# Performance work log

Measured on AMD Instinct MI355X. Metric: run time of the kernel, lower is better.

Reference implementation:

```python
import jax, jax.numpy as jnp
import numpy as np

B, T, N, K = 8, 1024, 64, 8


def _normalize_logprob(logmat, axis):
    # temperature = 1 in forward_backward
    norm = jax.scipy.special.logsumexp(logmat, axis=axis, keepdims=True)
    return logmat - norm, norm


def setup_inputs() -> dict:
    key = jax.random.key(0)
    k1, k2, k3 = jax.random.split(key, 3)
    log_a = jax.random.normal(k1, (B, T, N, K, K), dtype=jnp.float32)
    log_b = jax.random.normal(k2, (B, T, N, K), dtype=jnp.float32)
    logprob_z1 = jax.random.normal(k3, (N, K), dtype=jnp.float32)
    return {"log_a": log_a, "log_b": log_b, "logprob_z1": logprob_z1}


def reference(log_a, log_b, logprob_z1):
    # log_a: (B,T,N,K,K)  transition log-probs a[t][i,j] = p(z_t=i | z_{t-1}=j)
    # log_b: (B,T,N,K)    emission log-likelihoods
    # logprob_z1: (N,K)   initial state log-prob (Z_init parameter)
    b_tm = jnp.moveaxis(log_b, 1, 0)  # (T,B,N,K) time-major for scan
    a_tm = jnp.moveaxis(log_a, 1, 0)  # (T,B,N,K,K)

    # ---- forward recursion ----
    alpha0, norm0 = _normalize_logprob(logprob_z1[None] + log_b[:, 0], -1)  # (B,N,K),(B,N,1)

    def fstep(prev, xs):
        b_t, a_t = xs  # (B,N,K), (B,N,K,K)
        # alpha_t[i] = logsumexp_j( b_t[i] + a_t[i,j] + prev[j] )
        u = jax.scipy.special.logsumexp(
            b_t[..., :, None] + a_t + prev[..., None, :], axis=-1)
        alpha, nrm = _normalize_logprob(u, -1)
        return alpha, (alpha, nrm)

    _, (alphas, fnorms) = jax.lax.scan(fstep, alpha0, (b_tm[1:], a_tm[1:]))
    forward_probs = jnp.moveaxis(
        jnp.concatenate([alpha0[None], alphas], axis=0), 0, 1)  # (B,T,N,K)

    # ---- backward recursion ----
    betaT = jnp.zeros_like(alpha0)  # (B,N,K)

    def bstep(nxt, xs):
        b_tp1, a_tp1 = xs  # (B,N,K), (B,N,K,K)
        # beta_t[j] = logsumexp_i( nxt[i] + a_tp1[i,j] + b_tp1[i] )
        u = jax.scipy.special.logsumexp(
            nxt[..., :, None] + a_tp1 + b_tp1[..., :, None], axis=-2)
        beta, nrm = _normalize_logprob(u, -1)
        return beta, (beta, nrm)

    _, (betas, bnorms) = jax.lax.scan(
        bstep, betaT, (b_tm[1:], a_tm[1:]), reverse=True)
    backward_probs = jnp.moveaxis(
        jnp.concatenate([betas, betaT[None]], axis=0), 0, 1)  # (B,T,N,K)

    # ---- posteriors ----
    gamma1, _ = _normalize_logprob(forward_probs + backward_probs, -1)  # (B,T,N,K)

    # gamma2[t][i,j] ~ beta_t[i] + a_t[i,j] + b_t[i] + alpha_{t-1}[j], t >= 1
    g2u = (forward_probs[:, :-1, :, None, :]      # (B,T-1,N,1,K)
           + backward_probs[:, 1:, :, :, None]    # (B,T-1,N,K,1)
           + log_a[:, 1:]                         # (B,T-1,N,K,K)
           + log_b[:, 1:][..., None])             # (B,T-1,N,K,1)
    g2_norm = jax.scipy.special.logsumexp(g2u, axis=(-2, -1), keepdims=True)
    gamma2_unpad = g2u - g2_norm
    gamma2 = jnp.concatenate(
        [jnp.zeros_like(gamma2_unpad[:, :1]), gamma2_unpad], axis=1)  # (B,T,N,K,K)

    return forward_probs, backward_probs, gamma1, gamma2
```

## Files before the change

### kernel.cpp

```cpp
#include <hip/hip_runtime.h>

#define Tdim 1024
#define Ndim 64
#define FSZ (8 * 1024 * 64 * 8)

typedef unsigned uint2v __attribute__((ext_vector_type(2)));

#define DPPADD(v, ctrl) ((v) + __int_as_float(__builtin_amdgcn_update_dpp( \
    0, __float_as_int(v), ctrl, 0xF, 0xF, false)))

__device__ __forceinline__ float swap_add16(float v) {
  unsigned u = __float_as_uint(v);
  uint2v r = __builtin_amdgcn_permlane16_swap(u, u, false, false);
  return __uint_as_float(r[0]) + __uint_as_float(r[1]);
}
__device__ __forceinline__ float swap_add32(float v) {
  unsigned u = __float_as_uint(v);
  uint2v r = __builtin_amdgcn_permlane32_swap(u, u, false, false);
  return __uint_as_float(r[0]) + __uint_as_float(r[1]);
}

#define SUM_LO3(v) { v = DPPADD(v, 0xB1); v = DPPADD(v, 0x4E); v = DPPADD(v, 0x141); }
#define SUM_HI3(v) { v = DPPADD(v, 0x128); v = swap_add16(v); v = swap_add32(v); }

#define GLOAD_LDS(gp, lp) __builtin_amdgcn_global_load_lds( \
    (const __attribute__((address_space(1))) unsigned*)(gp), \
    (__attribute__((address_space(3))) unsigned*)(lp), 4, 0, 0)


__device__ __forceinline__ void stage_fwd(const float* __restrict__ a_base,
                                          const float* __restrict__ b_base,
                                          int t0, int swz, int lane,
                                          float* sA, float* sB) {
#pragma unroll
  for (int s = 0; s < 16; ++s) {
    int t = t0 + s; if (t > Tdim - 1) t = Tdim - 1;
    GLOAD_LDS(&a_base[(size_t)t * (Ndim * 64) + swz], &sA[s * 64]);
  }
#pragma unroll
  for (int h = 0; h < 2; ++h) {
    int tb = t0 + h * 8 + (lane >> 3); if (tb > Tdim - 1) tb = Tdim - 1;
    GLOAD_LDS(&b_base[(size_t)tb * (Ndim * 8) + (lane & 7)], &sB[h * 64]);
  }
}

__device__ __forceinline__ void stage_bwd(const float* __restrict__ a_base,
                                          const float* __restrict__ b_base,
                                          int t0, int swz, int lane,
                                          float* sA, float* sB) {
#pragma unroll
  for (int s = 0; s < 16; ++s) {
    int t = t0 - s; if (t < 0) t = 0;
    GLOAD_LDS(&a_base[(size_t)t * (Ndim * 64) + swz], &sA[s * 64]);
  }
#pragma unroll
  for (int h = 0; h < 2; ++h) {
    int tb = t0 - 1 - (h * 8 + (lane >> 3)); if (tb < 0) tb = 0;
    GLOAD_LDS(&b_base[(size_t)tb * (Ndim * 8) + (lane & 7)], &sB[h * 64]);
  }
}

__global__ __launch_bounds__(64, 1) void chains_kernel(const float* __restrict__ A,
                                                       const float* __restrict__ Bm,
                                                       const float* __restrict__ Z1,
                                                       float* __restrict__ Fout,
                                                       float* __restrict__ Bout) {
  __shared__ float sA0[1024], sA1[1024], sB0[128], sB1[128], sLa[128];
  const int lane = threadIdx.x;
  const int x = lane >> 3, y = lane & 7;
  const int swz = (x << 3) | (y ^ x);
  const int trw = (y << 3) | (x ^ y);
  const int chain = blockIdx.x & 511;
  const int b = chain >> 6, n = chain & 63;
  const size_t cbase = ((size_t)b * Tdim) * Ndim + n;
  const float* a_base = A + cbase * 64;
  const float* b_base = Bm + cbase * 8;

  if (blockIdx.x < 512) {
    float* f_base = Fout + cbase * 8;
    float v0 = Z1[n * 8 + y] + b_base[y];
    float q = __expf(v0);
    float T0 = q; SUM_LO3(T0);
    if (x == 0) f_base[y] = v0 - __logf(T0);
    float sc = __builtin_amdgcn_rcpf(T0);
    stage_fwd(a_base, b_base, 1, swz, lane, sA0, sB0);
#pragma unroll 1
    for (int kk = 0; kk < 64; ++kk) {
      const float* sA = (kk & 1) ? sA1 : sA0;
      const float* sB = (kk & 1) ? sB1 : sB0;
      float* nA = (kk & 1) ? sA0 : sA1;
      float* nB = (kk & 1) ? sB0 : sB1;
      const int t0 = 1 + kk * 16;
      float av[16], bv[16];
#pragma unroll
      for (int s = 0; s < 16; ++s) {
        av[s] = sA[s * 64 + ((s & 1) ? trw : swz)];
        bv[s] = sB[s * 8 + ((s & 1) ? y : x)];
      }
      __builtin_amdgcn_sched_barrier(0);
      if (kk + 1 < 64) stage_fwd(a_base, b_base, t0 + 16, swz, lane, nA, nB);
      __builtin_amdgcn_sched_barrier(0);
#pragma unroll
      for (int s = 0; s < 16; ++s) {
        int oidx = (s & 1) ? y : x;
        float v = __expf(av[s]) * q;
        if (!(s & 1)) { SUM_LO3(v); } else { SUM_HI3(v); }
        float S = v * (__expf(bv[s]) * sc);
        q = S;
        float T = S;
        if (!(s & 1)) { SUM_HI3(T); } else { SUM_LO3(T); }
        sc = __builtin_amdgcn_rcpf(T);
        float la = __logf(S * sc);
        if ((((s & 1) ? x : y)) == 0) sLa[s * 8 + oidx] = la;
      }
      __builtin_amdgcn_sched_barrier(0);
#pragma unroll
      for (int h = 0; h < 2; ++h) {
        int t = t0 + x + h * 8;
        if (t < Tdim) f_base[(size_t)t * (Ndim * 8) + y] = sLa[h * 64 + lane];
      }
    }
  } else {
    float* bo = Bout + cbase * 8;
    float bT = b_base[(size_t)(Tdim - 1) * (Ndim * 8) + x];
    float u = __expf(bT);
    if (x == 0) bo[(size_t)(Tdim - 1) * (Ndim * 8) + y] = 0.f;
    float sc = 1.0f;
    stage_bwd(a_base, b_base, Tdim - 1, swz, lane, sA0, sB0);
#pragma unroll 1
    for (int kk = 0; kk < 64; ++kk) {
      const float* sA = (kk & 1) ? sA1 : sA0;
      const float* sB = (kk & 1) ? sB1 : sB0;
      float* nA = (kk & 1) ? sA0 : sA1;
      float* nB = (kk & 1) ? sB0 : sB1;
      const int t0 = Tdim - 1 - kk * 16;
      float av[16], bv[16];
#pragma unroll
      for (int s = 0; s < 16; ++s) {
        av[s] = sA[s * 64 + ((s & 1) ? trw : swz)];
        bv[s] = sB[s * 8 + ((s & 1) ? x : y)];
      }
      __builtin_amdgcn_sched_barrier(0);
      if (kk + 1 < 64) stage_bwd(a_base, b_base, t0 - 16, swz, lane, nA, nB);
      __builtin_amdgcn_sched_barrier(0);
#pragma unroll
      for (int s = 0; s < 16; ++s) {
        float v = __expf(av[s]) * u;
        if (!(s & 1)) { SUM_HI3(v); } else { SUM_LO3(v); }
        int oidx = (s & 1) ? x : y;
        float unew = (__expf(bv[s]) * sc) * v;
        float W = v;
        if (!(s & 1)) { SUM_LO3(W); } else { SUM_HI3(W); }
        float scn = __builtin_amdgcn_rcpf(W);
        float lb = __logf(v * scn);
        if ((((s & 1) ? y : x)) == 0) sLa[s * 8 + oidx] = lb;
        u = unew;
        sc = scn;
      }
      __builtin_amdgcn_sched_barrier(0);
#pragma unroll
      for (int h = 0; h < 2; ++h) {
        int trow = t0 - (x + h * 8) - 1;
        if (trow >= 0) bo[(size_t)trow * (Ndim * 8) + y] = sLa[h * 64 + lane];
      }
    }
  }
}

__global__ __launch_bounds__(256) void gamma_kernel(const float* __restrict__ A,
                                                    const float* __restrict__ Bm,
                                                    const float* __restrict__ F,
                                                    const float* __restrict__ Bo,
                                                    float* __restrict__ G1,
                                                    float* __restrict__ G2) {
  const int lane = threadIdx.x & 63;
  const int i = lane & 7;
  const int gq = lane >> 3;
  const int g = (blockIdx.x * 4 + (threadIdx.x >> 6)) * 8 + gq;
  const int t = (g >> 6) & (Tdim - 1);

  const float bo_i = Bo[(size_t)g * 8 + i];

  {
    float u1 = F[(size_t)g * 8 + i] + bo_i;
    float s1 = __expf(u1);
    SUM_LO3(s1);
    G1[(size_t)g * 8 + i] = u1 - __logf(s1);
  }

  float4* o = (float4*)&G2[(size_t)g * 64 + i * 8];
  if (t == 0) {
    float4 z = make_float4(0.f, 0.f, 0.f, 0.f);
    o[0] = z; o[1] = z;
  } else {
    const float4* ap = (const float4*)&A[(size_t)g * 64 + i * 8];
    float4 a0 = ap[0], a1 = ap[1];
    const float4* fp = (const float4*)&F[((size_t)g - Ndim) * 8];
    float4 f0 = fp[0], f1 = fp[1];
    float c = bo_i + Bm[(size_t)g * 8 + i];
    float v0 = c + a0.x + f0.x, v1 = c + a0.y + f0.y;
    float v2 = c + a0.z + f0.z, v3 = c + a0.w + f0.w;
    float v4 = c + a1.x + f1.x, v5 = c + a1.y + f1.y;
    float v6 = c + a1.z + f1.z, v7 = c + a1.w + f1.w;
    float r = ((__expf(v0) + __expf(v1)) + (__expf(v2) + __expf(v3)))
            + ((__expf(v4) + __expf(v5)) + (__expf(v6) + __expf(v7)));
    SUM_LO3(r);
    float lq = __logf(r);
    o[0] = make_float4(v0 - lq, v1 - lq, v2 - lq, v3 - lq);
    o[1] = make_float4(v4 - lq, v5 - lq, v6 - lq, v7 - lq);
  }
}

extern "C" void kernel_launch(void* const* d_in, const int* in_sizes, int n_in,
                              void* d_out, int out_size, void* d_ws, size_t ws_size,
                              hipStream_t stream) {
  const float* A  = (const float*)d_in[0];
  const float* Bm = (const float*)d_in[1];
  const float* Z1 = (const float*)d_in[2];
  float* out = (float*)d_out;
  float* Fout = out;
  float* Bout = out + FSZ;
  float* G1   = out + 2 * FSZ;
  float* G2   = out + 3 * FSZ;

  chains_kernel<<<dim3(1024), dim3(64), 0, stream>>>(A, Bm, Z1, Fout, Bout);
  gamma_kernel<<<dim3(8 * Tdim * Ndim / 32), dim3(256), 0, stream>>>(A, Bm, Fout, Bout, G1, G2);
}
```

Baseline: 459.6 us.

## Defer chain rescaling off the critical path and widen gamma kernel threading

The forward and backward chains stop multiplying every step by the reciprocal of the row sum. They rescale only at two points per 16-step block, using a reciprocal computed two steps earlier, so the rcp no longer sits on the serial dependency chain. Log outputs are still normalized per step with a separate reciprocal. The backward loop adds a tau>=1 guard. The gamma kernel now gives each thread 4 outputs instead of 8, with 16 threads per group and twice as many blocks, and the DPP reductions are adjusted to match. The lazy scaling risks overflow or underflow across up to eight unnormalized steps, and the gamma change increases the thread count.

```diff
diff --git a/kernel.cpp b/kernel.cpp
--- a/kernel.cpp
+++ b/kernel.cpp
@@ -82,7 +82,7 @@
     float q = __expf(v0);
     float T0 = q; SUM_LO3(T0);
     if (x == 0) f_base[y] = v0 - __logf(T0);
-    float sc = __builtin_amdgcn_rcpf(T0);
+    q *= __builtin_amdgcn_rcpf(T0);
     stage_fwd(a_base, b_base, 1, swz, lane, sA0, sB0);
 #pragma unroll 1
     for (int kk = 0; kk < 64; ++kk) {
@@ -100,17 +100,19 @@
       __builtin_amdgcn_sched_barrier(0);
       if (kk + 1 < 64) stage_fwd(a_base, b_base, t0 + 16, swz, lane, nA, nB);
       __builtin_amdgcn_sched_barrier(0);
+      float scF = 1.0f;
 #pragma unroll
       for (int s = 0; s < 16; ++s) {
         int oidx = (s & 1) ? y : x;
         float v = __expf(av[s]) * q;
         if (!(s & 1)) { SUM_LO3(v); } else { SUM_HI3(v); }
-        float S = v * (__expf(bv[s]) * sc);
+        float S = v * __expf(bv[s]);
+        if (s == 7 || s == 15) S *= scF;
         q = S;
         float T = S;
         if (!(s & 1)) { SUM_HI3(T); } else { SUM_LO3(T); }
-        sc = __builtin_amdgcn_rcpf(T);
-        float la = __logf(S * sc);
+        if (s == 5 || s == 13) scF = __builtin_amdgcn_rcpf(T);
+        float la = __logf(S * __builtin_amdgcn_rcpf(T));
         if ((((s & 1) ? x : y)) == 0) sLa[s * 8 + oidx] = la;
       }
       __builtin_amdgcn_sched_barrier(0);
@@ -125,7 +127,6 @@
     float bT = b_base[(size_t)(Tdim - 1) * (Ndim * 8) + x];
     float u = __expf(bT);
     if (x == 0) bo[(size_t)(Tdim - 1) * (Ndim * 8) + y] = 0.f;
-    float sc = 1.0f;
     stage_bwd(a_base, b_base, Tdim - 1, swz, lane, sA0, sB0);
 #pragma unroll 1
     for (int kk = 0; kk < 64; ++kk) {
@@ -143,19 +144,23 @@
       __builtin_amdgcn_sched_barrier(0);
       if (kk + 1 < 64) stage_bwd(a_base, b_base, t0 - 16, swz, lane, nA, nB);
       __builtin_amdgcn_sched_barrier(0);
-#pragma unroll
-      for (int s = 0; s < 16; ++s) {
-        float v = __expf(av[s]) * u;
-        if (!(s & 1)) { SUM_HI3(v); } else { SUM_LO3(v); }
-        int oidx = (s & 1) ? x : y;
-        float unew = (__expf(bv[s]) * sc) * v;
-        float W = v;
-        if (!(s & 1)) { SUM_LO3(W); } else { SUM_HI3(W); }
-        float scn = __builtin_amdgcn_rcpf(W);
-        float lb = __logf(v * scn);
-        if ((((s & 1) ? y : x)) == 0) sLa[s * 8 + oidx] = lb;
-        u = unew;
-        sc = scn;
+      float scB = 1.0f;
+#pragma unroll
+      for (int s = 0; s < 16; ++s) {
+        int tau = t0 - s;
+        if (tau >= 1) {
+          float v = __expf(av[s]) * u;
+          if (!(s & 1)) { SUM_HI3(v); } else { SUM_LO3(v); }
+          int oidx = (s & 1) ? x : y;
+          float unew = __expf(bv[s]) * v;
+          if (s == 7 || s == 15) unew *= scB;
+          float W = v;
+          if (!(s & 1)) { SUM_LO3(W); } else { SUM_HI3(W); }
+          if (s == 5 || s == 13) scB = __builtin_amdgcn_rcpf(W);
+          float lb = __logf(v * __builtin_amdgcn_rcpf(W));
+          if ((((s & 1) ? y : x)) == 0) sLa[s * 8 + oidx] = lb;
+          u = unew;
+        }
       }
       __builtin_amdgcn_sched_barrier(0);
 #pragma unroll
@@ -173,10 +178,11 @@
                                                     const float* __restrict__ Bo,
                                                     float* __restrict__ G1,
                                                     float* __restrict__ G2) {
-  const int lane = threadIdx.x & 63;
-  const int i = lane & 7;
-  const int gq = lane >> 3;
-  const int g = (blockIdx.x * 4 + (threadIdx.x >> 6)) * 8 + gq;
+  const int tid = threadIdx.x;
+  const int lane16 = tid & 15;
+  const int i = (tid >> 1) & 7;
+  const int h = tid & 1;
+  const int g = blockIdx.x * 16 + (tid >> 4);
   const int t = (g >> 6) & (Tdim - 1);
 
   const float bo_i = Bo[(size_t)g * 8 + i];
@@ -184,30 +190,28 @@
   {
     float u1 = F[(size_t)g * 8 + i] + bo_i;
     float s1 = __expf(u1);
-    SUM_LO3(s1);
-    G1[(size_t)g * 8 + i] = u1 - __logf(s1);
-  }
-
-  float4* o = (float4*)&G2[(size_t)g * 64 + i * 8];
+    s1 = DPPADD(s1, 0x4E);
+    s1 = DPPADD(s1, 0x124);
+    s1 = DPPADD(s1, 0x128);
+    if (h == 0) G1[(size_t)g * 8 + i] = u1 - __logf(s1);
+  }
+
+  float4* o = (float4*)&G2[(size_t)g * 64 + lane16 * 4];
   if (t == 0) {
-    float4 z = make_float4(0.f, 0.f, 0.f, 0.f);
-    o[0] = z; o[1] = z;
+    *o = make_float4(0.f, 0.f, 0.f, 0.f);
   } else {
-    const float4* ap = (const float4*)&A[(size_t)g * 64 + i * 8];
-    float4 a0 = ap[0], a1 = ap[1];
-    const float4* fp = (const float4*)&F[((size_t)g - Ndim) * 8];
-    float4 f0 = fp[0], f1 = fp[1];
+    float4 a4 = *(const float4*)&A[(size_t)g * 64 + lane16 * 4];
+    float4 f4 = *(const float4*)&F[((size_t)g - Ndim) * 8 + h * 4];
     float c = bo_i + Bm[(size_t)g * 8 + i];
-    float v0 = c + a0.x + f0.x, v1 = c + a0.y + f0.y;
-    float v2 = c + a0.z + f0.z, v3 = c + a0.w + f0.w;
-    float v4 = c + a1.x + f1.x, v5 = c + a1.y + f1.y;
-    float v6 = c + a1.z + f1.z, v7 = c + a1.w + f1.w;
-    float r = ((__expf(v0) + __expf(v1)) + (__expf(v2) + __expf(v3)))
-            + ((__expf(v4) + __expf(v5)) + (__expf(v6) + __expf(v7)));
-    SUM_LO3(r);
+    float v0 = c + a4.x + f4.x, v1 = c + a4.y + f4.y;
+    float v2 = c + a4.z + f4.z, v3 = c + a4.w + f4.w;
+    float r = (__expf(v0) + __expf(v1)) + (__expf(v2) + __expf(v3));
+    r = DPPADD(r, 0xB1);
+    r = DPPADD(r, 0x4E);
+    r = DPPADD(r, 0x124);
+    r = DPPADD(r, 0x128);
     float lq = __logf(r);
-    o[0] = make_float4(v0 - lq, v1 - lq, v2 - lq, v3 - lq);
-    o[1] = make_float4(v4 - lq, v5 - lq, v6 - lq, v7 - lq);
+    *o = make_float4(v0 - lq, v1 - lq, v2 - lq, v3 - lq);
   }
 }
 
@@ -224,5 +228,5 @@
   float* G2   = out + 3 * FSZ;
 
   chains_kernel<<<dim3(1024), dim3(64), 0, stream>>>(A, Bm, Z1, Fout, Bout);
-  gamma_kernel<<<dim3(8 * Tdim * Ndim / 32), dim3(256), 0, stream>>>(A, Bm, Fout, Bout, G1, G2);
-}
+  gamma_kernel<<<dim3(8 * Tdim * Ndim / 16), dim3(256), 0, stream>>>(A, Bm, Fout, Bout, G1, G2);
+}
```

After: 458.9 us. Within noise of the previous version (-0.1%).
